# Performance work log

Measured on AMD Instinct MI355X. Metric: run time of the kernel, lower is better.

Reference implementation:

```python
import jax, jax.numpy as jnp
import numpy as np

N_NODES = 100000
N_EDGES = 1600000
D_FEAT = 64


def setup_inputs() -> dict:
    key = jax.random.key(0)
    k1, k2, k3 = jax.random.split(key, 3)
    x = jax.random.normal(k1, (N_NODES, D_FEAT), dtype=jnp.float32)
    edge_weight = jax.random.uniform(k2, (N_EDGES,), dtype=jnp.float32)
    edge_index = jax.random.randint(k3, (2, N_EDGES), 0, N_NODES, dtype=jnp.int64)
    return {"x": x, "edge_weight": edge_weight, "edge_index": edge_index}


def reference(x, edge_weight, edge_index):
    # GCNConv with lin.weight forced to identity, improved=False,
    # add_self_loops=True, normalize=True, bias=False.
    N = x.shape[0]
    row, col = edge_index[0], edge_index[1]  # source, target

    # add self loops with fill weight 1.0 (improved=False)
    loop = jnp.arange(N, dtype=edge_index.dtype)
    row = jnp.concatenate([row, loop])
    col = jnp.concatenate([col, loop])
    w = jnp.concatenate([edge_weight, jnp.ones((N,), dtype=x.dtype)])

    # symmetric GCN normalization: deg computed at target (col)
    deg = jax.ops.segment_sum(w, col, num_segments=N)
    deg_inv_sqrt = jnp.where(deg > 0, jax.lax.rsqrt(deg), 0.0)
    norm = deg_inv_sqrt[row] * w * deg_inv_sqrt[col]  # [E+N]

    # gather source features, weight, scatter-add to targets
    msg = x[row] * norm[:, None]                      # [E+N, F]
    out = jax.ops.segment_sum(msg, col, num_segments=N)
    return out
```

## Files before the change

kernel.cpp:

```cpp
#include <hip/hip_runtime.h>
#include <hip/hip_fp16.h>

constexpr int N_NODES = 100000;
constexpr int N_EDGES = 1600000;
constexpr int D_FEAT  = 64;
constexpr int STRIDE  = 48;

struct alignas(16) Half8 { __half2 h0, h1, h2, h3; };

__global__ void k_zero(unsigned long long* __restrict__ packed) {
    int i = blockIdx.x * blockDim.x + threadIdx.x;
    if (i < N_NODES) packed[i] = 0ull;
}

__global__ void k_hist(const float* __restrict__ ew, const int* __restrict__ row,
                       const int* __restrict__ col,
                       unsigned long long* __restrict__ packed,
                       unsigned int* __restrict__ ell) {
    int t = blockIdx.x * blockDim.x + threadIdx.x;
    if (t >= N_EDGES / 4) return;
    const int4   r4 = ((const int4*)row)[t];
    const int4   c4 = ((const int4*)col)[t];
    const float4 w4 = ((const float4*)ew)[t];

    unsigned long long a0 = (1ull << 32) | (unsigned long long)(unsigned int)(w4.x * 16777216.0f + 0.5f);
    unsigned long long a1 = (1ull << 32) | (unsigned long long)(unsigned int)(w4.y * 16777216.0f + 0.5f);
    unsigned long long a2 = (1ull << 32) | (unsigned long long)(unsigned int)(w4.z * 16777216.0f + 0.5f);
    unsigned long long a3 = (1ull << 32) | (unsigned long long)(unsigned int)(w4.w * 16777216.0f + 0.5f);

    unsigned long long o0 = atomicAdd(&packed[c4.x], a0);
    unsigned long long o1 = atomicAdd(&packed[c4.y], a1);
    unsigned long long o2 = atomicAdd(&packed[c4.z], a2);
    unsigned long long o3 = atomicAdd(&packed[c4.w], a3);

    int k0 = (int)(o0 >> 32), k1 = (int)(o1 >> 32);
    int k2 = (int)(o2 >> 32), k3 = (int)(o3 >> 32);

    unsigned int q0 = min((unsigned int)(w4.x * 32768.0f + 0.5f), 32767u);
    unsigned int q1 = min((unsigned int)(w4.y * 32768.0f + 0.5f), 32767u);
    unsigned int q2 = min((unsigned int)(w4.z * 32768.0f + 0.5f), 32767u);
    unsigned int q3 = min((unsigned int)(w4.w * 32768.0f + 0.5f), 32767u);

    if (k0 < STRIDE) ell[c4.x * STRIDE + k0] = ((unsigned int)r4.x << 15) | q0;
    if (k1 < STRIDE) ell[c4.y * STRIDE + k1] = ((unsigned int)r4.y << 15) | q1;
    if (k2 < STRIDE) ell[c4.z * STRIDE + k2] = ((unsigned int)r4.z << 15) | q2;
    if (k3 < STRIDE) ell[c4.w * STRIDE + k3] = ((unsigned int)r4.w << 15) | q3;
}

__global__ void k_dinv(const unsigned long long* __restrict__ packed,
                       float* __restrict__ dinv) {
    int i = blockIdx.x * blockDim.x + threadIdx.x;
    if (i < N_NODES) {
        float deg = (float)(unsigned int)(packed[i] & 0xffffffffu) * (1.0f / 16777216.0f);
        dinv[i] = rsqrtf(deg + 1.0f);
    }
}

__global__ void k_xprime(const float* __restrict__ x, const float* __restrict__ dinv,
                         __half* __restrict__ xh) {
    int t = blockIdx.x * blockDim.x + threadIdx.x;
    if (t >= N_NODES * (D_FEAT / 8)) return;
    int i = t >> 3;
    float di = dinv[i];
    const float4 f0 = ((const float4*)x)[2 * t];
    const float4 f1 = ((const float4*)x)[2 * t + 1];
    Half8 h;
    h.h0 = __float22half2_rn(make_float2(f0.x * di, f0.y * di));
    h.h1 = __float22half2_rn(make_float2(f0.z * di, f0.w * di));
    h.h2 = __float22half2_rn(make_float2(f1.x * di, f1.y * di));
    h.h3 = __float22half2_rn(make_float2(f1.z * di, f1.w * di));
    ((Half8*)xh)[t] = h;
}

__global__ void k_gather(const __half* __restrict__ xh, const float* __restrict__ dinv,
                         const unsigned int* __restrict__ ell,
                         const unsigned long long* __restrict__ packed,
                         float* __restrict__ out) {
    long long gid = (long long)blockIdx.x * blockDim.x + threadIdx.x;
    int node = (int)(gid >> 6);
    if (node >= N_NODES) return;
    int lane = (int)(gid & 63);
    int sub  = lane >> 3;
    int q    = lane & 7;

    int n = min((int)(packed[node] >> 32), STRIDE);
    const unsigned int* base = ell + (size_t)node * STRIDE;

    float4 acc0 = make_float4(0.f, 0.f, 0.f, 0.f);
    float4 acc1 = make_float4(0.f, 0.f, 0.f, 0.f);
    int k = sub;
    for (; k + 8 < n; k += 16) {
        unsigned int ea = base[k];
        unsigned int eb = base[k + 8];
        int ra = (int)(ea >> 15), rb = (int)(eb >> 15);
        float sa = (float)(ea & 0x7fffu) * (1.0f / 32768.0f);
        float sb = (float)(eb & 0x7fffu) * (1.0f / 32768.0f);
        Half8 ha = ((const Half8*)(xh + (size_t)ra * D_FEAT))[q];
        Half8 hb = ((const Half8*)(xh + (size_t)rb * D_FEAT))[q];
        float2 a0 = __half22float2(ha.h0), a1 = __half22float2(ha.h1);
        float2 a2 = __half22float2(ha.h2), a3 = __half22float2(ha.h3);
        float2 b0 = __half22float2(hb.h0), b1 = __half22float2(hb.h1);
        float2 b2 = __half22float2(hb.h2), b3 = __half22float2(hb.h3);
        acc0.x = fmaf(sa, a0.x, acc0.x); acc0.y = fmaf(sa, a0.y, acc0.y);
        acc0.z = fmaf(sa, a1.x, acc0.z); acc0.w = fmaf(sa, a1.y, acc0.w);
        acc1.x = fmaf(sa, a2.x, acc1.x); acc1.y = fmaf(sa, a2.y, acc1.y);
        acc1.z = fmaf(sa, a3.x, acc1.z); acc1.w = fmaf(sa, a3.y, acc1.w);
        acc0.x = fmaf(sb, b0.x, acc0.x); acc0.y = fmaf(sb, b0.y, acc0.y);
        acc0.z = fmaf(sb, b1.x, acc0.z); acc0.w = fmaf(sb, b1.y, acc0.w);
        acc1.x = fmaf(sb, b2.x, acc1.x); acc1.y = fmaf(sb, b2.y, acc1.y);
        acc1.z = fmaf(sb, b3.x, acc1.z); acc1.w = fmaf(sb, b3.y, acc1.w);
    }
    if (k < n) {
        unsigned int e = base[k];
        int r = (int)(e >> 15);
        float s = (float)(e & 0x7fffu) * (1.0f / 32768.0f);
        Half8 hv = ((const Half8*)(xh + (size_t)r * D_FEAT))[q];
        float2 v0 = __half22float2(hv.h0), v1 = __half22float2(hv.h1);
        float2 v2 = __half22float2(hv.h2), v3 = __half22float2(hv.h3);
        acc0.x = fmaf(s, v0.x, acc0.x); acc0.y = fmaf(s, v0.y, acc0.y);
        acc0.z = fmaf(s, v1.x, acc0.z); acc0.w = fmaf(s, v1.y, acc0.w);
        acc1.x = fmaf(s, v2.x, acc1.x); acc1.y = fmaf(s, v2.y, acc1.y);
        acc1.z = fmaf(s, v3.x, acc1.z); acc1.w = fmaf(s, v3.y, acc1.w);
    }

    acc0.x += __shfl_xor(acc0.x, 8); acc0.x += __shfl_xor(acc0.x, 16); acc0.x += __shfl_xor(acc0.x, 32);
    acc0.y += __shfl_xor(acc0.y, 8); acc0.y += __shfl_xor(acc0.y, 16); acc0.y += __shfl_xor(acc0.y, 32);
    acc0.z += __shfl_xor(acc0.z, 8); acc0.z += __shfl_xor(acc0.z, 16); acc0.z += __shfl_xor(acc0.z, 32);
    acc0.w += __shfl_xor(acc0.w, 8); acc0.w += __shfl_xor(acc0.w, 16); acc0.w += __shfl_xor(acc0.w, 32);
    acc1.x += __shfl_xor(acc1.x, 8); acc1.x += __shfl_xor(acc1.x, 16); acc1.x += __shfl_xor(acc1.x, 32);
    acc1.y += __shfl_xor(acc1.y, 8); acc1.y += __shfl_xor(acc1.y, 16); acc1.y += __shfl_xor(acc1.y, 32);
    acc1.z += __shfl_xor(acc1.z, 8); acc1.z += __shfl_xor(acc1.z, 16); acc1.z += __shfl_xor(acc1.z, 32);
    acc1.w += __shfl_xor(acc1.w, 8); acc1.w += __shfl_xor(acc1.w, 16); acc1.w += __shfl_xor(acc1.w, 32);

    if (sub == 0) {
        float di = dinv[node];
        Half8 hs = ((const Half8*)(xh + (size_t)node * D_FEAT))[q];
        float2 s0 = __half22float2(hs.h0), s1 = __half22float2(hs.h1);
        float2 s2 = __half22float2(hs.h2), s3 = __half22float2(hs.h3);
        float4 o0, o1;
        o0.x = di * (acc0.x + s0.x);
        o0.y = di * (acc0.y + s0.y);
        o0.z = di * (acc0.z + s1.x);
        o0.w = di * (acc0.w + s1.y);
        o1.x = di * (acc1.x + s2.x);
        o1.y = di * (acc1.y + s2.y);
        o1.z = di * (acc1.z + s3.x);
        o1.w = di * (acc1.w + s3.y);
        float4* orow = (float4*)(out + (size_t)node * D_FEAT);
        orow[2 * q]     = o0;
        orow[2 * q + 1] = o1;
    }
}

extern "C" void kernel_launch(void* const* d_in, const int* in_sizes, int n_in,
                              void* d_out, int out_size, void* d_ws, size_t ws_size,
                              hipStream_t stream) {
    const float* x   = (const float*)d_in[0];
    const float* ew  = (const float*)d_in[1];
    const int*   ei  = (const int*)d_in[2];
    const int*   row = ei;
    const int*   col = ei + N_EDGES;
    float* out = (float*)d_out;

    char* ws = (char*)d_ws;
    unsigned long long* packed = (unsigned long long*)(ws);
    float*        dinv = (float*)(ws + 800000);
    unsigned int* ell  = (unsigned int*)(ws + 1200000);
    __half*       xh   = (__half*)(ws + 20400000);

    const int B = 256;

    k_zero<<<(N_NODES + B - 1) / B, B, 0, stream>>>(packed);
    k_hist<<<(N_EDGES / 4 + B - 1) / B, B, 0, stream>>>(ew, row, col, packed, ell);
    k_dinv<<<(N_NODES + B - 1) / B, B, 0, stream>>>(packed, dinv);
    k_xprime<<<(N_NODES * (D_FEAT / 8) + B - 1) / B, B, 0, stream>>>(x, dinv, xh);

    long long total_threads = (long long)N_NODES * 64;
    k_gather<<<(int)((total_threads + B - 1) / B), B, 0, stream>>>(
        xh, dinv, ell, packed, out);
}
```

Before: 264.5 us.

## Split histogram atomics from ELL placement into separate kernel passes

The histogram kernel now only does the packed atomic adds and writes each edge's slot rank as a byte into a scratch buffer. A new placement kernel rereads row, col and weight plus the ranks and writes the ELL entries. Taking the dependent scattered stores out of the atomic kernel is meant to reduce how long atomic latency stalls it. In exchange the edge arrays are read twice and one extra launch is added. The rank buffer shares workspace with the half-precision feature buffer, which is only written after placement has finished.

```diff
diff --git a/kernel.cpp b/kernel.cpp
--- a/kernel.cpp
+++ b/kernel.cpp
@@ -13,13 +13,11 @@
     if (i < N_NODES) packed[i] = 0ull;
 }
 
-__global__ void k_hist(const float* __restrict__ ew, const int* __restrict__ row,
-                       const int* __restrict__ col,
+__global__ void k_hist(const float* __restrict__ ew, const int* __restrict__ col,
                        unsigned long long* __restrict__ packed,
-                       unsigned int* __restrict__ ell) {
+                       uchar4* __restrict__ rank4) {
     int t = blockIdx.x * blockDim.x + threadIdx.x;
     if (t >= N_EDGES / 4) return;
-    const int4   r4 = ((const int4*)row)[t];
     const int4   c4 = ((const int4*)col)[t];
     const float4 w4 = ((const float4*)ew)[t];
 
@@ -33,18 +31,8 @@
     unsigned long long o2 = atomicAdd(&packed[c4.z], a2);
     unsigned long long o3 = atomicAdd(&packed[c4.w], a3);
 
-    int k0 = (int)(o0 >> 32), k1 = (int)(o1 >> 32);
-    int k2 = (int)(o2 >> 32), k3 = (int)(o3 >> 32);
-
-    unsigned int q0 = min((unsigned int)(w4.x * 32768.0f + 0.5f), 32767u);
-    unsigned int q1 = min((unsigned int)(w4.y * 32768.0f + 0.5f), 32767u);
-    unsigned int q2 = min((unsigned int)(w4.z * 32768.0f + 0.5f), 32767u);
-    unsigned int q3 = min((unsigned int)(w4.w * 32768.0f + 0.5f), 32767u);
-
-    if (k0 < STRIDE) ell[c4.x * STRIDE + k0] = ((unsigned int)r4.x << 15) | q0;
-    if (k1 < STRIDE) ell[c4.y * STRIDE + k1] = ((unsigned int)r4.y << 15) | q1;
-    if (k2 < STRIDE) ell[c4.z * STRIDE + k2] = ((unsigned int)r4.z << 15) | q2;
-    if (k3 < STRIDE) ell[c4.w * STRIDE + k3] = ((unsigned int)r4.w << 15) | q3;
+    rank4[t] = make_uchar4((unsigned char)(o0 >> 32), (unsigned char)(o1 >> 32),
+                           (unsigned char)(o2 >> 32), (unsigned char)(o3 >> 32));
 }
 
 __global__ void k_dinv(const unsigned long long* __restrict__ packed,
@@ -56,8 +44,30 @@
     }
 }
 
-__global__ void k_xprime(const float* __restrict__ x, const float* __restrict__ dinv,
-                         __half* __restrict__ xh) {
+__global__ void k_place(const int* __restrict__ row, const int* __restrict__ col,
+                        const float* __restrict__ ew,
+                        const uchar4* __restrict__ rank4,
+                        unsigned int* __restrict__ ell) {
+    int t = blockIdx.x * blockDim.x + threadIdx.x;
+    if (t >= N_EDGES / 4) return;
+    const int4   r4 = ((const int4*)row)[t];
+    const int4   c4 = ((const int4*)col)[t];
+    const float4 w4 = ((const float4*)ew)[t];
+    const uchar4 k4 = rank4[t];
+
+    unsigned int q0 = min((unsigned int)(w4.x * 32768.0f + 0.5f), 32767u);
+    unsigned int q1 = min((unsigned int)(w4.y * 32768.0f + 0.5f), 32767u);
+    unsigned int q2 = min((unsigned int)(w4.z * 32768.0f + 0.5f), 32767u);
+    unsigned int q3 = min((unsigned int)(w4.w * 32768.0f + 0.5f), 32767u);
+
+    if (k4.x < STRIDE) ell[c4.x * STRIDE + k4.x] = ((unsigned int)r4.x << 15) | q0;
+    if (k4.y < STRIDE) ell[c4.y * STRIDE + k4.y] = ((unsigned int)r4.y << 15) | q1;
+    if (k4.z < STRIDE) ell[c4.z * STRIDE + k4.z] = ((unsigned int)r4.z << 15) | q2;
+    if (k4.w < STRIDE) ell[c4.w * STRIDE + k4.w] = ((unsigned int)r4.w << 15) | q3;
+}
+
+__global__ void k_convert(const float* __restrict__ x, const float* __restrict__ dinv,
+                          __half* __restrict__ xh) {
     int t = blockIdx.x * blockDim.x + threadIdx.x;
     if (t >= N_NODES * (D_FEAT / 8)) return;
     int i = t >> 3;
@@ -164,16 +174,18 @@
 
     char* ws = (char*)d_ws;
     unsigned long long* packed = (unsigned long long*)(ws);
-    float*        dinv = (float*)(ws + 800000);
-    unsigned int* ell  = (unsigned int*)(ws + 1200000);
-    __half*       xh   = (__half*)(ws + 20400000);
+    float*        dinv  = (float*)(ws + 800000);
+    unsigned int* ell   = (unsigned int*)(ws + 1200000);
+    __half*       xh    = (__half*)(ws + 20400000);
+    uchar4*       rank4 = (uchar4*)(ws + 20400000);
 
     const int B = 256;
 
     k_zero<<<(N_NODES + B - 1) / B, B, 0, stream>>>(packed);
-    k_hist<<<(N_EDGES / 4 + B - 1) / B, B, 0, stream>>>(ew, row, col, packed, ell);
+    k_hist<<<(N_EDGES / 4 + B - 1) / B, B, 0, stream>>>(ew, col, packed, rank4);
     k_dinv<<<(N_NODES + B - 1) / B, B, 0, stream>>>(packed, dinv);
-    k_xprime<<<(N_NODES * (D_FEAT / 8) + B - 1) / B, B, 0, stream>>>(x, dinv, xh);
+    k_place<<<(N_EDGES / 4 + B - 1) / B, B, 0, stream>>>(row, col, ew, rank4, ell);
+    k_convert<<<(N_NODES * (D_FEAT / 8) + B - 1) / B, B, 0, stream>>>(x, dinv, xh);
 
     long long total_threads = (long long)N_NODES * 64;
     k_gather<<<(int)((total_threads + B - 1) / B), B, 0, stream>>>(
```

After: 231.2 us. 1.14x faster.
